# Kernel optimization log

Measured on AMD Instinct MI355X. Metric: run time of the kernel, lower is better.

## Reference

```python
import jax, jax.numpy as jnp
import numpy as np

B, N, G = 16, 4096, 1024
D1, D2 = 128, 256          # feature1 / feature2 channels
C_IN = D1 + D2             # 384
C_H, C_OUT = 256, 256
BN_EPS = 1e-5


def setup_inputs() -> dict:
    key = jax.random.key(0)
    ks = jax.random.split(key, 10)
    inp = {
        "feature1": jax.random.normal(ks[0], (B, D1, N), jnp.float32),
        "coord1": jax.random.normal(ks[1], (B, 3, N), jnp.float32),
        "feature2": jax.random.normal(ks[2], (B, D2, G), jnp.float32),
        "coord2": jax.random.normal(ks[3], (B, 3, G), jnp.float32),
        # conv1x1 + BN params, layer 1: 384 -> 256
        "W1": jax.random.normal(ks[4], (C_H, C_IN), jnp.float32) / np.sqrt(C_IN),
        "b1": jnp.zeros((C_H,), jnp.float32),
        "gamma1": jnp.ones((C_H,), jnp.float32),
        "beta1": jnp.zeros((C_H,), jnp.float32),
        # layer 2: 256 -> 256
        "W2": jax.random.normal(ks[5], (C_OUT, C_H), jnp.float32) / np.sqrt(C_H),
        "b2": jnp.zeros((C_OUT,), jnp.float32),
        "gamma2": jnp.ones((C_OUT,), jnp.float32),
        "beta2": jnp.zeros((C_OUT,), jnp.float32),
    }
    return inp


def _conv_bn_relu(x, W, b, gamma, beta):
    # x: [B, C_in, N]; 1x1 conv == channel GEMM
    y = jnp.einsum('oi,bin->bon', W, x) + b[None, :, None]
    m = y.mean(axis=(0, 2), keepdims=True)           # BN1d train-mode batch stats
    v = y.var(axis=(0, 2), keepdims=True)
    y = (y - m) * jax.lax.rsqrt(v + BN_EPS) * gamma[None, :, None] + beta[None, :, None]
    return jax.nn.relu(y)


def reference(feature1, coord1, feature2, coord2,
              W1, b1, gamma1, beta1, W2, b2, gamma2, beta2):
    c1 = jnp.transpose(coord1, (0, 2, 1))    # [B, N, 3]
    c2 = jnp.transpose(coord2, (0, 2, 1))    # [B, G, 3]
    f2 = jnp.transpose(feature2, (0, 2, 1))  # [B, G, D2]

    # squared pairwise distances [B, N, G]
    d = (jnp.sum(c1 * c1, -1)[:, :, None]
         + jnp.sum(c2 * c2, -1)[:, None, :]
         - 2.0 * jnp.einsum('bnd,bgd->bng', c1, c2))

    # 3 nearest neighbors (smallest distances)
    neg_d, idx = jax.lax.top_k(-d, 3)        # [B, N, 3]
    dists = -neg_d
    recip = 1.0 / (dists + 1e-8)
    weight = recip / jnp.sum(recip, axis=-1, keepdims=True)  # [B, N, 3]

    # gather neighbor features: [B, N, 3, D2]
    gathered = jnp.take_along_axis(f2[:, None, :, :], idx[:, :, :, None], axis=2)
    interp = jnp.sum(gathered * weight[..., None], axis=2)   # [B, N, D2]

    feat = jnp.concatenate([jnp.transpose(feature1, (0, 2, 1)), interp], axis=-1)
    x = jnp.transpose(feat, (0, 2, 1))       # [B, 384, N]

    x = _conv_bn_relu(x, W1, b1, gamma1, beta1)
    x = _conv_bn_relu(x, W2, b2, gamma2, beta2)
    return x
```

## Files before the change

### kernel.cpp

```cpp
#include <hip/hip_runtime.h>

#define DEVI __device__ __forceinline__

typedef unsigned short u16;
typedef unsigned int   u32;
typedef u16  u16x8 __attribute__((ext_vector_type(8)));
typedef u16  u16x4 __attribute__((ext_vector_type(4)));
typedef short bf16x8 __attribute__((ext_vector_type(8)));
typedef float f32x4 __attribute__((ext_vector_type(4)));

static constexpr int BB = 16, NN = 4096, GG = 1024;
static constexpr int D1 = 128, D2 = 256, CIN = 384, CH = 256;

DEVI float bf2f(u16 h) { u32 u = ((u32)h) << 16; float f; __builtin_memcpy(&f, &u, 4); return f; }
DEVI u16 f2bf(float f) {
    u32 u; __builtin_memcpy(&u, &f, 4);
    u32 r = (u + 0x7fffu + ((u >> 16) & 1u)) >> 16;
    return (u16)r;
}

DEVI void gload16(const void* g, void* l) {
    __builtin_amdgcn_global_load_lds((const __attribute__((address_space(1))) void*)g,
                                     (__attribute__((address_space(3))) void*)l, 16, 0, 0);
}

__global__ void k_convw(const float* __restrict__ W1, const float* __restrict__ W2,
                        u16* __restrict__ W1b, u16* __restrict__ W2b) {
    int i = blockIdx.x * 256 + threadIdx.x;
    if (i < CH * CIN) W1b[i] = f2bf(W1[i]);
    int j = i - CH * CIN;
    if (j >= 0 && j < CH * CH) W2b[j] = f2bf(W2[j]);
}

__global__ void k_f2t(const float* __restrict__ f2, u16* __restrict__ f2t) {
    int b = blockIdx.z, ct = blockIdx.y, gt = blockIdx.x;
    __shared__ u16 tile[64][65];
    int t = threadIdx.x; int g = t & 63; int q = t >> 6;
    for (int p = 0; p < 16; ++p) {
        int cl = p * 4 + q;
        tile[g][cl] = f2bf(f2[((size_t)(b * D2 + ct * 64 + cl)) * GG + gt * 64 + g]);
    }
    __syncthreads();
    for (int p = 0; p < 16; ++p) {
        int gl = p * 4 + q;
        f2t[((size_t)(b * GG + gt * 64 + gl)) * D2 + ct * 64 + g] = tile[gl][g];
    }
}

__global__ __launch_bounds__(256) void k_knn(const float* __restrict__ c1, const float* __restrict__ c2,
                                             int* __restrict__ idxo, float* __restrict__ wo) {
    int b = blockIdx.y; int t = threadIdx.x;
    int q = t >> 2, s = t & 3;
    int n = blockIdx.x * 64 + q;
    __shared__ float4 sp[GG];
    __shared__ int mi[256][4];
    const float* cb = c2 + (size_t)b * 3 * GG;
    for (int i = t; i < GG; i += 256) {
        float x = cb[i], y = cb[GG + i], z = cb[2 * GG + i];
        sp[i] = make_float4(x, y, z, x * x + y * y + z * z);
    }
    __syncthreads();
    const float* pb = c1 + (size_t)b * 3 * NN;
    float px = pb[n], py = pb[NN + n], pz = pb[2 * NN + n];
    float pn = px * px + py * py + pz * pz;
    float d0 = 3.4e38f, d1 = 3.4e38f, d2 = 3.4e38f, d3 = 3.4e38f;
    int i0 = 0, i1 = 0, i2 = 0, i3 = 0;
    for (int gb = 0; gb < GG; gb += 16) {
        #pragma unroll
        for (int u = 0; u < 4; ++u) {
            int g = gb + u * 4 + s;
            float4 p = sp[g];
            float d = pn + p.w - 2.f * (px * p.x + py * p.y + pz * p.z);
            if (d < d3) {
                if (d < d2) {
                    d3 = d2; i3 = i2;
                    if (d < d1) {
                        d2 = d1; i2 = i1;
                        if (d < d0) { d1 = d0; i1 = i0; d0 = d; i0 = g; }
                        else { d1 = d; i1 = g; }
                    } else { d2 = d; i2 = g; }
                } else { d3 = d; i3 = g; }
            }
        }
    }
    mi[t][0] = i0; mi[t][1] = i1; mi[t][2] = i2; mi[t][3] = i3;
    __syncthreads();
    if (s == 0) {
        double e0 = 1e300, e1 = 1e300, e2 = 1e300;
        int j0 = 0x7fffffff, j1 = 0x7fffffff, j2 = 0x7fffffff;
        #pragma unroll 4
        for (int k = 0; k < 16; ++k) {
            int g = mi[q * 4 + (k >> 2)][k & 3];
            float4 p = sp[g];
            double dx = (double)px - (double)p.x;
            double dy = (double)py - (double)p.y;
            double dz = (double)pz - (double)p.z;
            double d = dx * dx + dy * dy + dz * dz;
            bool lt2 = d < e2 || (d == e2 && g < j2);
            if (lt2) {
                bool lt1 = d < e1 || (d == e1 && g < j1);
                if (lt1) {
                    e2 = e1; j2 = j1;
                    bool lt0 = d < e0 || (d == e0 && g < j0);
                    if (lt0) { e1 = e0; j1 = j0; e0 = d; j0 = g; }
                    else { e1 = d; j1 = g; }
                } else { e2 = d; j2 = g; }
            }
        }
        float r0 = 1.f / ((float)e0 + 1e-8f);
        float r1 = 1.f / ((float)e1 + 1e-8f);
        float r2 = 1.f / ((float)e2 + 1e-8f);
        float sum = r0 + r1 + r2;
        size_t base = ((size_t)b * NN + n) * 3;
        idxo[base] = j0; idxo[base + 1] = j1; idxo[base + 2] = j2;
        wo[base] = r0 / sum; wo[base + 1] = r1 / sum; wo[base + 2] = r2 / sum;
    }
}

__global__ void k_pack(const float* __restrict__ f1, const u16* __restrict__ f2t,
                       const int* __restrict__ idxo, const float* __restrict__ wo,
                       u16* __restrict__ Xp) {
    int b = blockIdx.y; int n0 = blockIdx.x * 64;
    __shared__ u16 Xt[64][392];
    int t = threadIdx.x; int j = t & 63; int q = t >> 6;
    for (int p = 0; p < 4; ++p) {
        int oct = p * 4 + q; int cb = oct * 8;
        u16x8 o;
        #pragma unroll
        for (int k = 0; k < 8; ++k)
            o[k] = f2bf(f1[((size_t)(b * D1 + cb + k)) * NN + n0 + j]);
        *(u16x8*)&Xt[j][cb] = o;
    }
    size_t bn = (size_t)b * NN + n0 + j;
    int g0 = idxo[bn * 3], g1 = idxo[bn * 3 + 1], g2 = idxo[bn * 3 + 2];
    float w0 = wo[bn * 3], w1 = wo[bn * 3 + 1], w2 = wo[bn * 3 + 2];
    const u16* r0 = f2t + ((size_t)b * GG + g0) * D2;
    const u16* r1 = f2t + ((size_t)b * GG + g1) * D2;
    const u16* r2 = f2t + ((size_t)b * GG + g2) * D2;
    for (int p = 0; p < 8; ++p) {
        int oct = p * 4 + q; int cb = oct * 8;
        u16x8 a = *(const u16x8*)(r0 + cb);
        u16x8 bb = *(const u16x8*)(r1 + cb);
        u16x8 cc = *(const u16x8*)(r2 + cb);
        u16x8 o;
        #pragma unroll
        for (int k = 0; k < 8; ++k)
            o[k] = f2bf(w0 * bf2f(a[k]) + w1 * bf2f(bb[k]) + w2 * bf2f(cc[k]));
        *(u16x8*)&Xt[j][D1 + cb] = o;
    }
    __syncthreads();
    u16* dst = Xp + ((size_t)b * NN + n0) * CIN;
    for (int p = 0; p < 12; ++p) {
        int ci = p * 256 + t;
        int row = ci / 48, ch = ci % 48;
        *(u16x8*)(dst + (size_t)ci * 8) = *(const u16x8*)&Xt[row][ch * 8];
    }
}

template<int K>
__global__ __launch_bounds__(256) void k_gemm(const u16* __restrict__ A, const u16* __restrict__ Bm,
                                              const float* __restrict__ bias, u16* __restrict__ Yp,
                                              float* __restrict__ S1, float* __restrict__ S2) {
    int nt = blockIdx.x, mt = blockIdx.y, b = blockIdx.z;
    int c0 = mt * 128; size_t n0 = (size_t)b * NN + nt * 128;
    __shared__ u16 Al[128 * 32], Bl[128 * 32];
    __shared__ float sred[4][64], qred[4][64];
    int t = threadIdx.x, lane = t & 63, w = t >> 6;
    int wr = w >> 1, wc = w & 1;
    f32x4 acc[4][4];
    #pragma unroll
    for (int m = 0; m < 4; ++m)
        #pragma unroll
        for (int n = 0; n < 4; ++n) acc[m][n] = (f32x4){0.f, 0.f, 0.f, 0.f};
    int lr = w * 32 + (lane >> 2);
    int lc = (lane & 3) * 8;
    for (int ks = 0; ks < K / 32; ++ks) {
        __syncthreads();
        #pragma unroll
        for (int i = 0; i < 2; ++i) {
            gload16(A + (size_t)(c0 + lr + i * 16) * K + ks * 32 + lc, Al + (w * 32 + i * 16) * 32);
            gload16(Bm + (n0 + lr + i * 16) * K + ks * 32 + lc, Bl + (w * 32 + i * 16) * 32);
        }
        __syncthreads();
        bf16x8 af[4], bfr[4];
        #pragma unroll
        for (int m = 0; m < 4; ++m)
            af[m] = *(const bf16x8*)&Al[(wr * 64 + m * 16 + (lane & 15)) * 32 + (lane >> 4) * 8];
        #pragma unroll
        for (int n = 0; n < 4; ++n)
            bfr[n] = *(const bf16x8*)&Bl[(wc * 64 + n * 16 + (lane & 15)) * 32 + (lane >> 4) * 8];
        #pragma unroll
        for (int m = 0; m < 4; ++m)
            #pragma unroll
            for (int n = 0; n < 4; ++n)
                acc[m][n] = __builtin_amdgcn_mfma_f32_16x16x32_bf16(af[m], bfr[n], acc[m][n], 0, 0, 0);
    }
    float sacc[4][4], qacc[4][4];
    #pragma unroll
    for (int m = 0; m < 4; ++m) {
        int c = c0 + wr * 64 + m * 16 + (lane >> 4) * 4;
        float b0 = bias[c], b1 = bias[c + 1], b2 = bias[c + 2], b3 = bias[c + 3];
        #pragma unroll
        for (int j = 0; j < 4; ++j) { sacc[m][j] = 0.f; qacc[m][j] = 0.f; }
        #pragma unroll
        for (int n = 0; n < 4; ++n) {
            size_t nn = n0 + wc * 64 + n * 16 + (lane & 15);
            f32x4 v = acc[m][n];
            float y0 = v[0] + b0, y1 = v[1] + b1, y2 = v[2] + b2, y3 = v[3] + b3;
            u16x4 o;
            o[0] = f2bf(y0); o[1] = f2bf(y1); o[2] = f2bf(y2); o[3] = f2bf(y3);
            *(u16x4*)(Yp + nn * CH + c) = o;
            sacc[m][0] += y0; qacc[m][0] += y0 * y0;
            sacc[m][1] += y1; qacc[m][1] += y1 * y1;
            sacc[m][2] += y2; qacc[m][2] += y2 * y2;
            sacc[m][3] += y3; qacc[m][3] += y3 * y3;
        }
    }
    #pragma unroll
    for (int m = 0; m < 4; ++m)
        #pragma unroll
        for (int j = 0; j < 4; ++j) {
            float s = sacc[m][j], qv = qacc[m][j];
            #pragma unroll
            for (int mask = 1; mask <= 8; mask <<= 1) {
                s  += __shfl_xor(s, mask);
                qv += __shfl_xor(qv, mask);
            }
            sacc[m][j] = s; qacc[m][j] = qv;
        }
    int g = lane >> 4;
    if ((lane & 15) == 0) {
        #pragma unroll
        for (int m = 0; m < 4; ++m)
            #pragma unroll
            for (int j = 0; j < 4; ++j) {
                sred[w][m * 16 + g * 4 + j] = sacc[m][j];
                qred[w][m * 16 + g * 4 + j] = qacc[m][j];
            }
    }
    __syncthreads();
    if (t < 128) {
        int half = t >> 6, cl = t & 63;
        float s  = sred[half * 2][cl] + sred[half * 2 + 1][cl];
        float qv = qred[half * 2][cl] + qred[half * 2 + 1][cl];
        atomicAdd(&S1[c0 + half * 64 + cl], s);
        atomicAdd(&S2[c0 + half * 64 + cl], qv);
    }
}

__global__ void k_fin(const float* __restrict__ S1, const float* __restrict__ S2,
                      const float* __restrict__ gamma, const float* __restrict__ beta,
                      float* __restrict__ scale, float* __restrict__ shift) {
    int c = threadIdx.x;
    float inv = 1.f / 65536.f;
    float m = S1[c] * inv;
    float v = S2[c] * inv - m * m;
    float sc = gamma[c] * rsqrtf(v + 1e-5f);
    scale[c] = sc; shift[c] = beta[c] - m * sc;
}

__global__ void k_bnrelu(const u16* __restrict__ Y, const float* __restrict__ scale,
                         const float* __restrict__ shift, u16* __restrict__ X2) {
    __shared__ float sc[256], sh[256];
    int t = threadIdx.x;
    sc[t] = scale[t]; sh[t] = shift[t];
    __syncthreads();
    size_t i = ((size_t)blockIdx.x * 256 + t) * 8;
    int c = (int)(i & 255);
    u16x8 v = *(const u16x8*)(Y + i);
    u16x8 o;
    #pragma unroll
    for (int k = 0; k < 8; ++k) {
        float f = fmaxf(sc[c + k] * bf2f(v[k]) + sh[c + k], 0.f);
        o[k] = f2bf(f);
    }
    *(u16x8*)(X2 + i) = o;
}

__global__ void k_final(const u16* __restrict__ Y2, const float* __restrict__ scale,
                        const float* __restrict__ shift, float* __restrict__ out) {
    int b = blockIdx.y, n0 = blockIdx.x * 64;
    __shared__ u16 tile[64 * 256];
    __shared__ float sc[256], sh[256];
    int t = threadIdx.x;
    sc[t] = scale[t]; sh[t] = shift[t];
    #pragma unroll
    for (int p = 0; p < 8; ++p) {
        int r = p * 8 + (t >> 5); int o = t & 31;
        u16x8 v = *(const u16x8*)(Y2 + ((size_t)(b * NN + n0 + r)) * CH + o * 8);
        int osw = o ^ (r & 7);
        *(u16x8*)&tile[r * 256 + osw * 8] = v;
    }
    __syncthreads();
    for (int p = 0; p < 64; ++p) {
        int c = p * 4 + (t >> 6); int n = t & 63;
        int osw = (c >> 3) ^ (n & 7);
        float f = bf2f(tile[n * 256 + osw * 8 + (c & 7)]);
        out[((size_t)(b * CH + c)) * NN + n0 + n] = fmaxf(sc[c] * f + sh[c], 0.f);
    }
}

extern "C" void kernel_launch(void* const* d_in, const int* in_sizes, int n_in,
                              void* d_out, int out_size, void* d_ws, size_t ws_size,
                              hipStream_t stream) {
    const float* f1  = (const float*)d_in[0];
    const float* c1  = (const float*)d_in[1];
    const float* f2  = (const float*)d_in[2];
    const float* c2  = (const float*)d_in[3];
    const float* W1  = (const float*)d_in[4];
    const float* b1  = (const float*)d_in[5];
    const float* g1  = (const float*)d_in[6];
    const float* be1 = (const float*)d_in[7];
    const float* W2  = (const float*)d_in[8];
    const float* b2  = (const float*)d_in[9];
    const float* g2  = (const float*)d_in[10];
    const float* be2 = (const float*)d_in[11];
    float* out = (float*)d_out;
    char* ws = (char*)d_ws;

    u16* Xp    = (u16*)(ws);
    u16* Y1p   = (u16*)(ws + 50331648);
    u16* X2p   = Xp;
    u16* Y2p   = Y1p;
    u16* W1b   = (u16*)(ws + 83886080);
    u16* W2b   = (u16*)(ws + 84082688);
    u16* F2t   = (u16*)(ws + 84213760);
    int*  idxo = (int*)(ws + 92602368);
    float* wo  = (float*)(ws + 93388800);
    float* stats = (float*)(ws + 94175232);
    float* S1a = stats,        *S2a = stats + 256;
    float* S1b = stats + 512,  *S2b = stats + 768;
    float* sc1 = stats + 1024, *sh1 = stats + 1280;
    float* sc2 = stats + 1536, *sh2 = stats + 1792;

    hipMemsetAsync(stats, 0, 4096, stream);
    k_convw<<<640, 256, 0, stream>>>(W1, W2, W1b, W2b);
    k_f2t<<<dim3(16, 4, 16), 256, 0, stream>>>(f2, F2t);
    k_knn<<<dim3(64, 16), 256, 0, stream>>>(c1, c2, idxo, wo);
    k_pack<<<dim3(64, 16), 256, 0, stream>>>(f1, F2t, idxo, wo, Xp);
    k_gemm<CIN><<<dim3(32, 2, 16), 256, 0, stream>>>(W1b, Xp, b1, Y1p, S1a, S2a);
    k_fin<<<1, 256, 0, stream>>>(S1a, S2a, g1, be1, sc1, sh1);
    k_bnrelu<<<8192, 256, 0, stream>>>(Y1p, sc1, sh1, X2p);
    k_gemm<CH><<<dim3(32, 2, 16), 256, 0, stream>>>(W2b, X2p, b2, Y2p, S1b, S2b);
    k_fin<<<1, 256, 0, stream>>>(S1b, S2b, g2, be2, sc2, sh2);
    k_final<<<dim3(64, 16), 256, 0, stream>>>(Y2p, sc2, sh2, out);
}
```

Before: 287.0 us.

## Double-buffer GEMM LDS tiles and make kNN top-4 insertion branchless

The GEMM kernel now keeps two LDS buffers and prefetches the next K-slice with global_load_lds while MFMAs consume the current one. This replaces two barriers per iteration with one and hides global latency behind compute. The kNN scan replaces its nested-branch top-4 insertion with predicated selects, which avoids wavefront divergence at the cost of executing every update unconditionally. Correctness of the double buffer depends on async LDS loads having completed by the time the single barrier is reached.

```diff
diff --git a/kernel.cpp b/kernel.cpp
--- a/kernel.cpp
+++ b/kernel.cpp
@@ -70,17 +70,13 @@
         for (int u = 0; u < 4; ++u) {
             int g = gb + u * 4 + s;
             float4 p = sp[g];
-            float d = pn + p.w - 2.f * (px * p.x + py * p.y + pz * p.z);
-            if (d < d3) {
-                if (d < d2) {
-                    d3 = d2; i3 = i2;
-                    if (d < d1) {
-                        d2 = d1; i2 = i1;
-                        if (d < d0) { d1 = d0; i1 = i0; d0 = d; i0 = g; }
-                        else { d1 = d; i1 = g; }
-                    } else { d2 = d; i2 = g; }
-                } else { d3 = d; i3 = g; }
-            }
+            float dot = px * p.x + py * p.y + pz * p.z;
+            float d = pn + p.w - 2.f * dot;
+            bool c0 = d < d0, c1 = d < d1, c2 = d < d2, c3 = d < d3;
+            d3 = c2 ? d2 : (c3 ? d : d3);  i3 = c2 ? i2 : (c3 ? g : i3);
+            d2 = c1 ? d1 : (c2 ? d : d2);  i2 = c1 ? i1 : (c2 ? g : i2);
+            d1 = c0 ? d0 : (c1 ? d : d1);  i1 = c0 ? i0 : (c1 ? g : i1);
+            d0 = c0 ? d  : d0;             i0 = c0 ? g : i0;
         }
     }
     mi[t][0] = i0; mi[t][1] = i1; mi[t][2] = i2; mi[t][3] = i3;
@@ -161,9 +157,10 @@
 __global__ __launch_bounds__(256) void k_gemm(const u16* __restrict__ A, const u16* __restrict__ Bm,
                                               const float* __restrict__ bias, u16* __restrict__ Yp,
                                               float* __restrict__ S1, float* __restrict__ S2) {
+    constexpr int NK = K / 32;
     int nt = blockIdx.x, mt = blockIdx.y, b = blockIdx.z;
     int c0 = mt * 128; size_t n0 = (size_t)b * NN + nt * 128;
-    __shared__ u16 Al[128 * 32], Bl[128 * 32];
+    __shared__ u16 Al[2][128 * 32], Bl[2][128 * 32];
     __shared__ float sred[4][64], qred[4][64];
     int t = threadIdx.x, lane = t & 63, w = t >> 6;
     int wr = w >> 1, wc = w & 1;
@@ -174,26 +171,36 @@
         for (int n = 0; n < 4; ++n) acc[m][n] = (f32x4){0.f, 0.f, 0.f, 0.f};
     int lr = w * 32 + (lane >> 2);
     int lc = (lane & 3) * 8;
-    for (int ks = 0; ks < K / 32; ++ks) {
-        __syncthreads();
-        #pragma unroll
-        for (int i = 0; i < 2; ++i) {
-            gload16(A + (size_t)(c0 + lr + i * 16) * K + ks * 32 + lc, Al + (w * 32 + i * 16) * 32);
-            gload16(Bm + (n0 + lr + i * 16) * K + ks * 32 + lc, Bl + (w * 32 + i * 16) * 32);
-        }
-        __syncthreads();
+
+    #pragma unroll
+    for (int i = 0; i < 2; ++i) {
+        gload16(A + (size_t)(c0 + lr + i * 16) * K + lc, &Al[0][(w * 32 + i * 16) * 32]);
+        gload16(Bm + (n0 + lr + i * 16) * K + lc, &Bl[0][(w * 32 + i * 16) * 32]);
+    }
+    __syncthreads();
+
+    for (int ks = 0; ks < NK; ++ks) {
+        int cur = ks & 1;
+        if (ks + 1 < NK) {
+            #pragma unroll
+            for (int i = 0; i < 2; ++i) {
+                gload16(A + (size_t)(c0 + lr + i * 16) * K + (ks + 1) * 32 + lc, &Al[cur ^ 1][(w * 32 + i * 16) * 32]);
+                gload16(Bm + (n0 + lr + i * 16) * K + (ks + 1) * 32 + lc, &Bl[cur ^ 1][(w * 32 + i * 16) * 32]);
+            }
+        }
         bf16x8 af[4], bfr[4];
         #pragma unroll
         for (int m = 0; m < 4; ++m)
-            af[m] = *(const bf16x8*)&Al[(wr * 64 + m * 16 + (lane & 15)) * 32 + (lane >> 4) * 8];
+            af[m] = *(const bf16x8*)&Al[cur][(wr * 64 + m * 16 + (lane & 15)) * 32 + (lane >> 4) * 8];
         #pragma unroll
         for (int n = 0; n < 4; ++n)
-            bfr[n] = *(const bf16x8*)&Bl[(wc * 64 + n * 16 + (lane & 15)) * 32 + (lane >> 4) * 8];
+            bfr[n] = *(const bf16x8*)&Bl[cur][(wc * 64 + n * 16 + (lane & 15)) * 32 + (lane >> 4) * 8];
         #pragma unroll
         for (int m = 0; m < 4; ++m)
             #pragma unroll
             for (int n = 0; n < 4; ++n)
                 acc[m][n] = __builtin_amdgcn_mfma_f32_16x16x32_bf16(af[m], bfr[n], acc[m][n], 0, 0, 0);
+        __syncthreads();
     }
     float sacc[4][4], qacc[4][4];
     #pragma unroll
```

Measured after the change: 292.2 us. About the same (+1.8%).
